# Optimization experiments

Hardware: AMD Instinct MI355X
Metric: run time of the kernel (lower is better)

Reference implementation:

```python
import jax, jax.numpy as jnp
import numpy as np

TIMESTEPS = 8
NUM_HEADS = 16
CTX = 1024
D = 1024
HD = D // NUM_HEADS
LN_EPS = 1e-5


def setup_inputs() -> dict:
    key = jax.random.key(0)
    ks = jax.random.split(key, 16)
    s = 0.02
    return {
        "current_embs": jax.random.normal(ks[0], (4, CTX, D), jnp.float32),
        "emb_table": jax.random.normal(ks[1], (TIMESTEPS, D), jnp.float32) * s,
        "Wq": jax.random.normal(ks[2], (NUM_HEADS, D, HD), jnp.float32) * s,
        "Wk": jax.random.normal(ks[3], (NUM_HEADS, D, HD), jnp.float32) * s,
        "Wv": jax.random.normal(ks[4], (NUM_HEADS, D, HD), jnp.float32) * s,
        "fc_w": jax.random.normal(ks[5], (D, D), jnp.float32) * s,
        "fc_b": jnp.zeros((D,), jnp.float32),
        "ln1_w": jnp.ones((D,), jnp.float32),
        "ln1_b": jnp.zeros((D,), jnp.float32),
        "ln2_w": jnp.ones((D,), jnp.float32),
        "ln2_b": jnp.zeros((D,), jnp.float32),
        "mlp_w1": jax.random.normal(ks[6], (D, 2 * D), jnp.float32) * s,
        "mlp_b1": jnp.zeros((2 * D,), jnp.float32),
        "mlp_w2": jax.random.normal(ks[7], (2 * D, D), jnp.float32) * s,
        "mlp_b2": jnp.zeros((D,), jnp.float32),
        "mlp_w3": jax.random.normal(ks[8], (D, D), jnp.float32) * s,
        "mlp_b3": jnp.zeros((D,), jnp.float32),
    }


def _layernorm(x, w, b):
    mu = jnp.mean(x, axis=-1, keepdims=True)
    var = jnp.var(x, axis=-1, keepdims=True)
    return (x - mu) * jax.lax.rsqrt(var + LN_EPS) * w + b


def _block(x, Wq, Wk, Wv, fc_w, fc_b, ln1_w, ln1_b, ln2_w, ln2_b,
           mlp_w1, mlp_b1, mlp_w2, mlp_b2, mlp_w3, mlp_b3):
    B, T, C = x.shape
    h = _layernorm(x, ln1_w, ln1_b)
    # per-head projections: [B,H,T,HD]
    q = jnp.einsum("btd,hdk->bhtk", h, Wq)
    k = jnp.einsum("btd,hdk->bhtk", h, Wk)
    v = jnp.einsum("btd,hdk->bhtk", h, Wv)
    # NOTE: original scales by embed_size**-0.5 (C), not head_dim**-0.5
    wei = jnp.einsum("bhtk,bhsk->bhts", q, k) * (C ** -0.5)
    causal = jnp.tril(jnp.ones((T, T), bool))
    wei = jnp.where(causal, wei, -jnp.inf)
    wei = jax.nn.softmax(wei, axis=-1)
    attn = jnp.einsum("bhts,bhsk->bhtk", wei, v)  # [B,H,T,HD]
    attn = attn.transpose(0, 2, 1, 3).reshape(B, T, C)  # concat heads
    sa = attn @ fc_w + fc_b
    x = x + sa  # dropout is identity in eval mode
    h2 = _layernorm(x, ln2_w, ln2_b)
    m = ((h2 @ mlp_w1 + mlp_b1) @ mlp_w2 + mlp_b2) @ mlp_w3 + mlp_b3
    m = jax.nn.gelu(m, approximate=False)  # GELU after three stacked Linears, as in source
    return x + m


def reference(current_embs, emb_table, Wq, Wk, Wv, fc_w, fc_b,
              ln1_w, ln1_b, ln2_w, ln2_b,
              mlp_w1, mlp_b1, mlp_w2, mlp_b2, mlp_w3, mlp_b3):
    new_embs = current_embs
    for i in range(TIMESTEPS):
        current_embs = current_embs + new_embs + emb_table[i][None, None, :]
        new_embs = _block(current_embs, Wq, Wk, Wv, fc_w, fc_b,
                          ln1_w, ln1_b, ln2_w, ln2_b,
                          mlp_w1, mlp_b1, mlp_w2, mlp_b2, mlp_w3, mlp_b3)
    return new_embs
```

## Files before the change

kernel.cpp:

```cpp
#include <hip/hip_runtime.h>
#include <hip/hip_bf16.h>
#include <math.h>

typedef __bf16 bf16;
typedef __bf16 bf16x8 __attribute__((ext_vector_type(8)));
typedef __bf16 bf16x4 __attribute__((ext_vector_type(4)));
typedef short  s16x4  __attribute__((ext_vector_type(4)));
typedef float  f32x4  __attribute__((ext_vector_type(4)));

#define MFMA32(a,b,c) __builtin_amdgcn_mfma_f32_16x16x32_bf16((a),(b),(c),0,0,0)
#define MFMA16(a,b,c) __builtin_amdgcn_mfma_f32_16x16x16bf16_1k((a),(b),(c),0,0,0)
#define EXP2F(x) __builtin_amdgcn_exp2f(x)
#define GLL16(gp, lp) __builtin_amdgcn_global_load_lds(\
    (const __attribute__((address_space(1))) void*)(gp), \
    (__attribute__((address_space(3))) void*)(lp), 16, 0, 0)

__device__ __forceinline__ float wave_sum(float v){
#pragma unroll
  for(int off=1; off<64; off<<=1) v += __shfl_xor(v, off);
  return v;
}

__global__ __launch_bounds__(256) void add_ln_kernel(
    const float* __restrict__ xsrc, const float* __restrict__ addsrc,
    const float* __restrict__ emb,
    const float* __restrict__ gw, const float* __restrict__ gb,
    float* __restrict__ xout, bf16* __restrict__ hout)
{
  const int row = blockIdx.x;
  const int t = threadIdx.x;
  const size_t rbase = (size_t)row * 1024;
  float4 x = ((const float4*)(xsrc + rbase))[t];
  if(addsrc){
    float4 a = ((const float4*)(addsrc + rbase))[t];
    x.x += a.x; x.y += a.y; x.z += a.z; x.w += a.w;
  }
  if(emb){
    float4 e = ((const float4*)emb)[t];
    x.x += e.x; x.y += e.y; x.z += e.z; x.w += e.w;
  }
  if(xout) ((float4*)(xout + rbase))[t] = x;

  float s = x.x + x.y + x.z + x.w;
  float q = x.x*x.x + x.y*x.y + x.z*x.z + x.w*x.w;
  s = wave_sum(s); q = wave_sum(q);
  __shared__ float red[8];
  const int w = t >> 6;
  if((t & 63) == 0){ red[w] = s; red[4+w] = q; }
  __syncthreads();
  s = red[0]+red[1]+red[2]+red[3];
  q = red[4]+red[5]+red[6]+red[7];
  const float mean = s * (1.0f/1024.0f);
  const float var  = q * (1.0f/1024.0f) - mean*mean;
  const float inv  = rsqrtf(var + 1e-5f);

  float4 wv = ((const float4*)gw)[t];
  float4 bv = ((const float4*)gb)[t];
  bf16x4 hv;
  hv[0] = (bf16)((x.x - mean)*inv*wv.x + bv.x);
  hv[1] = (bf16)((x.y - mean)*inv*wv.y + bv.y);
  hv[2] = (bf16)((x.z - mean)*inv*wv.z + bv.z);
  hv[3] = (bf16)((x.w - mean)*inv*wv.w + bv.w);
  *(bf16x4*)(hout + rbase + t*4) = hv;
}

__global__ __launch_bounds__(256) void pack_all_kernel(
    const float* __restrict__ Wq, const float* __restrict__ Wk, const float* __restrict__ Wv,
    const float* __restrict__ fcw, const float* __restrict__ w2,
    const float* __restrict__ w3,  const float* __restrict__ w1,
    bf16* __restrict__ wqkvT, bf16* __restrict__ fcT,
    bf16* __restrict__ w2T,   bf16* __restrict__ w3T, bf16* __restrict__ w1pl)
{
  const int bid = blockIdx.x;
  const int tid = threadIdx.x;
  if(bid >= 1792){
    const int i0 = (bid-1792)*2048 + tid*8;
    float4 a = *(const float4*)(w1 + i0);
    float4 b = *(const float4*)(w1 + i0 + 4);
    bf16x8 o;
    o[0]=(bf16)a.x; o[1]=(bf16)a.y; o[2]=(bf16)a.z; o[3]=(bf16)a.w;
    o[4]=(bf16)b.x; o[5]=(bf16)b.y; o[6]=(bf16)b.z; o[7]=(bf16)b.w;
    *(bf16x8*)(w1pl + i0) = o;
    return;
  }

  __shared__ float tile[64][65];
  const float* src; bf16* dst;
  int src_ld, dst_ld;
  if(bid < 768){
    const int seg = bid >> 8, r8 = bid & 255;
    const int h = r8 >> 4, d0 = (r8 & 15)*64;
    const float* W = (seg==0) ? Wq : (seg==1 ? Wk : Wv);
    src = W + h*65536 + (size_t)d0*64;  src_ld = 64;
    dst = wqkvT + ((size_t)(seg*1024 + h*64))*1024 + d0;  dst_ld = 1024;
  } else if(bid < 1024){
    const int t2 = bid - 768;
    const int k0 = (t2 >> 4)*64, n0 = (t2 & 15)*64;
    src = fcw + (size_t)k0*1024 + n0;  src_ld = 1024;
    dst = fcT + (size_t)n0*1024 + k0;  dst_ld = 1024;
  } else if(bid < 1536){
    const int t2 = bid - 1024;
    const int k0 = (t2 >> 4)*64, n0 = (t2 & 15)*64;
    src = w2 + (size_t)k0*1024 + n0;  src_ld = 1024;
    dst = w2T + (size_t)n0*2048 + k0;  dst_ld = 2048;
  } else {
    const int t2 = bid - 1536;
    const int k0 = (t2 >> 4)*64, n0 = (t2 & 15)*64;
    src = w3 + (size_t)k0*1024 + n0;  src_ld = 1024;
    dst = w3T + (size_t)n0*1024 + k0;  dst_ld = 1024;
  }

  {
    const int r = tid >> 4, c4 = (tid & 15)*4;
#pragma unroll
    for(int p=0; p<4; p++){
      float4 v = *(const float4*)(src + (size_t)(r + 16*p)*src_ld + c4);
      tile[r+16*p][c4]   = v.x;
      tile[r+16*p][c4+1] = v.y;
      tile[r+16*p][c4+2] = v.z;
      tile[r+16*p][c4+3] = v.w;
    }
  }
  __syncthreads();
  {
    const int n = tid >> 2, k16 = (tid & 3)*16;
#pragma unroll
    for(int half=0; half<2; half++){
      bf16x8 o;
#pragma unroll
      for(int j=0; j<8; j++) o[j] = (bf16)tile[k16 + half*8 + j][n];
      *(bf16x8*)(dst + (size_t)n*dst_ld + k16 + half*8) = o;
    }
  }
}

__global__ __launch_bounds__(256) void biasmv_kernel(const float* __restrict__ bin, const bf16* __restrict__ WT,
                                                     const float* __restrict__ badd, float* __restrict__ out, int Kd){
  const int n = blockIdx.x, t = threadIdx.x;
  float acc = 0.f;
  for(int k=t; k<Kd; k+=256) acc += bin[k]*(float)WT[(size_t)n*Kd + k];
  acc = wave_sum(acc);
  __shared__ float red[4];
  if((t&63)==0) red[t>>6] = acc;
  __syncthreads();
  if(t==0) out[n] = red[0]+red[1]+red[2]+red[3] + badd[n];
}

template<int EPI, int BLKM, int KH>
__global__ __launch_bounds__(256,2) void gemm_kernel(
    const bf16* __restrict__ A, const bf16* __restrict__ Bt,
    float* __restrict__ outf, bf16* __restrict__ outb,
    bf16* __restrict__ o2, bf16* __restrict__ o3,
    const float* __restrict__ bias, const float* __restrict__ res,
    const float* __restrict__ res2, const float* __restrict__ embn,
    int N, int K)
{
  constexpr int RM = BLKM/32;
  constexpr int HM = BLKM/2;
  constexpr int AISS = BLKM/32;
  __shared__ __align__(16) bf16 As[KH*BLKM*64];
  __shared__ __align__(16) bf16 Bs[KH*128*64];
  const int tid = threadIdx.x, w = tid>>6, lane = tid&63;
  const int quad = lane>>4, l16 = lane&15;
  const int wm = w&1, wn = w>>1;
  const int tn = blockIdx.x, tm = blockIdx.y;

  const int srow = lane>>3;
  const int sch  = (lane&7) ^ srow;
  const bf16* Ag = A  + (size_t)(tm*BLKM + w*8 + srow)*K + sch*8;
  const bf16* Bg = Bt + (size_t)(tn*128  + w*8 + srow)*K + sch*8;

  f32x4 acc[RM][4] = {};

  for(int k0 = 0; k0 < K; k0 += 64*KH){
#pragma unroll
    for(int h=0; h<KH; h++){
#pragma unroll
      for(int i=0;i<AISS;i++) GLL16(Ag + h*64 + (size_t)(i*32)*K, As + h*(BLKM*64) + (w*8 + i*32)*64);
#pragma unroll
      for(int i=0;i<4;i++)    GLL16(Bg + h*64 + (size_t)(i*32)*K, Bs + h*(128*64) + (w*8 + i*32)*64);
    }
    Ag += 64*KH; Bg += 64*KH;
    __syncthreads();
#pragma unroll
    for(int h=0; h<KH; h++){
      const bf16* Ash = As + h*(BLKM*64);
      const bf16* Bsh = Bs + h*(128*64);
      bf16x8 af[RM][2], bfr[4][2];
#pragma unroll
      for(int r=0;r<RM;r++){
        const int row = wm*HM + r*16 + l16;
        const bf16* rp = Ash + row*64;
#pragma unroll
        for(int kc=0;kc<2;kc++)
          af[r][kc] = *(const bf16x8*)(rp + ((kc*4+quad) ^ (row&7))*8);
      }
#pragma unroll
      for(int c=0;c<4;c++){
        const int row = wn*64 + c*16 + l16;
        const bf16* rp = Bsh + row*64;
#pragma unroll
        for(int kc=0;kc<2;kc++)
          bfr[c][kc] = *(const bf16x8*)(rp + ((kc*4+quad) ^ (row&7))*8);
      }
#pragma unroll
      for(int kc=0;kc<2;kc++)
#pragma unroll
        for(int r=0;r<RM;r++)
#pragma unroll
          for(int c=0;c<4;c++)
            acc[r][c] = MFMA32(af[r][kc], bfr[c][kc], acc[r][c]);
    }
    __syncthreads();
  }

#pragma unroll
  for(int r=0;r<RM;r++){
    const int grow0 = tm*BLKM + wm*HM + r*16 + quad*4;
#pragma unroll
    for(int c=0;c<4;c++){
      const int gcol = tn*128 + wn*64 + c*16 + l16;
      float bv = 0.0f;
      if constexpr (EPI>=1 && EPI!=4) bv = bias[gcol];
      if constexpr (EPI==4){
        const int seg = gcol >> 10;
        if(seg < 2){
          bf16* op = (seg==0) ? outb : o2;
          const float qs = (seg==0) ? 0.045084439f : 1.0f;
          const int col = gcol & 1023;
#pragma unroll
          for(int g=0; g<4; g++)
            op[(size_t)(grow0+g)*1024 + col] = (bf16)(acc[r][c][g]*qs);
        } else {
          const int col0 = gcol & 1023, hh = col0>>6, kk = col0&63;
          const int btok = grow0>>10, t0 = grow0&1023;
          bf16x4 pv;
#pragma unroll
          for(int g=0; g<4; g++) pv[g] = (bf16)acc[r][c][g];
          *(bf16x4*)(o3 + ((size_t)(btok*16+hh)*64 + kk)*1024 + t0) = pv;
        }
      } else {
        const float ev = (EPI==5) ? embn[gcol] : 0.0f;
#pragma unroll
        for(int g=0; g<4; g++){
          const float vv = acc[r][c][g] + bv;
          const size_t idx = (size_t)(grow0+g)*N + gcol;
          if constexpr (EPI<=1){
            outb[idx] = (bf16)vv;
          } else if constexpr (EPI==2){
            outf[idx] = res[idx] + vv;
          } else if constexpr (EPI==3){
            const float gel = 0.5f*vv*(1.0f + erff(vv*0.70710678118654752f));
            outf[idx] = res[idx] + gel;
          } else {
            const float gel = 0.5f*vv*(1.0f + erff(vv*0.70710678118654752f));
            outf[idx] = res[idx] + gel + res2[idx] + ev;
          }
        }
      }
    }
  }
}

constexpr int KSZ = 64*64;

__global__ __launch_bounds__(256,4) void attn_kernel(
    const bf16* __restrict__ Q, const bf16* __restrict__ Km,
    const bf16* __restrict__ Vt, bf16* __restrict__ O)
{
  __shared__ __align__(16) bf16 Ks[2*KSZ];
  __shared__ __align__(16) bf16 Vs[2*KSZ];
  const int qt = (int)((0xCDEF98BA67453210ull >> (blockIdx.y*4)) & 15);
  const int bh = blockIdx.x;
  const int b = bh >> 4, h = bh & 15;
  const int tid = threadIdx.x;
  const int w = tid>>6, lane = tid&63, quad = lane>>4, l16 = lane&15;
  const size_t qbase = (size_t)b*1024*1024 + (size_t)h*64;
  const size_t vbase = (size_t)(bh*64)*1024;
  const int qrow0 = qt*64 + w*16;
  const int myrow = qrow0 + l16;

  const bf16* qp = Q + qbase + (size_t)myrow*1024 + quad*8;
  bf16x8 bq0 = *(const bf16x8*)qp, bq1 = *(const bf16x8*)(qp + 32);

  f32x4 o[4] = {};
  float l = 0.f;
  const f32x4 zf = {0.f,0.f,0.f,0.f};

  const bf16* kg = Km + qbase + (size_t)(w*8 + (lane>>3))*1024 + ((lane&7)^(lane>>3))*8;
  const bf16* vg = Vt + vbase + (size_t)(w*8 + (lane>>3))*1024 + ((lane&7)^(lane>>3))*8;

  GLL16(kg,                       Ks + w*512);
  GLL16(kg + (size_t)32*1024,     Ks + 2048 + w*512);
  GLL16(vg,                       Vs + w*512);
  GLL16(vg + (size_t)32*1024,     Vs + 2048 + w*512);

  for(int kb = 0; kb <= qt; kb++){
    const int cur = kb & 1;
    __syncthreads();

    if(kb < qt){
      const bf16* kgp = kg + (size_t)(kb+1)*64*1024;
      const bf16* vgp = vg + (size_t)(kb+1)*64;
      bf16* kd = Ks + (cur^1)*KSZ + w*512;
      bf16* vd = Vs + (cur^1)*KSZ + w*512;
      GLL16(kgp,                   kd);
      GLL16(kgp + (size_t)32*1024, kd + 2048);
      GLL16(vgp,                   vd);
      GLL16(vgp + (size_t)32*1024, vd + 2048);
    }

    const bool diag = (kb == qt);
    const int nc = diag ? (w+1) : 4;
    const bf16* ksb = Ks + cur*KSZ;
    const bf16* vsb = Vs + cur*KSZ;

    f32x4 s[4];
#pragma unroll
    for(int c=0;c<4;c++){
      if(c >= nc) continue;
      const int row = c*16 + l16;
      const bf16* rp = ksb + row*64;
      bf16x8 ak0 = *(const bf16x8*)(rp + (( quad      ^ (row&7))<<3));
      bf16x8 ak1 = *(const bf16x8*)(rp + (((quad^4)   ^ (row&7))<<3));
      s[c] = MFMA32(ak0, bq0, zf);
      s[c] = MFMA32(ak1, bq1, s[c]);
    }

    s16x4 pp[4];
#pragma unroll
    for(int c=0;c<4;c++){
      if(c >= nc) continue;
      bf16x4 pb;
#pragma unroll
      for(int g=0;g<4;g++){
        const int key = kb*64 + c*16 + quad*4 + g;
        const float e = (diag && key > myrow) ? 0.f : EXP2F(s[c][g]);
        l += e; pb[g] = (bf16)e;
      }
      pp[c] = __builtin_bit_cast(s16x4, pb);
    }

#pragma unroll
    for(int c=0;c<4;c++){
      if(c >= nc) continue;
#pragma unroll
      for(int d=0;d<4;d++){
        const int row = d*16 + l16;
        const int eo  = ((((c*2 + (quad>>1)) ^ (row&7))<<3) + ((quad&1)<<2));
        bf16x4 av = *(const bf16x4*)(vsb + row*64 + eo);
        o[d] = MFMA16(__builtin_bit_cast(s16x4, av), pp[c], o[d]);
      }
    }
  }

  l += __shfl_xor(l, 16); l += __shfl_xor(l, 32);

  __syncthreads();
  {
    bf16* ot = Ks + w*(16*72);
    const float inv = 1.0f / l;
#pragma unroll
    for(int d=0;d<4;d++)
#pragma unroll
      for(int g=0;g<4;g++)
        ot[l16*72 + d*16 + quad*4 + g] = (bf16)(o[d][g]*inv);
#pragma unroll
    for(int p2=0;p2<2;p2++){
      const int qr = (lane>>3) + 8*p2, hd0 = (lane&7)*8;
      bf16x8 val = *(const bf16x8*)(ot + qr*72 + hd0);
      *(bf16x8*)(O + qbase + (size_t)(qrow0+qr)*1024 + hd0) = val;
    }
  }
}

extern "C" void kernel_launch(void* const* d_in, const int* in_sizes, int n_in,
                              void* d_out, int out_size, void* d_ws, size_t ws_size,
                              hipStream_t stream)
{
  const float* x_in = (const float*)d_in[0];
  const float* emb  = (const float*)d_in[1];
  const float* Wq   = (const float*)d_in[2];
  const float* Wk   = (const float*)d_in[3];
  const float* Wv   = (const float*)d_in[4];
  const float* fcw  = (const float*)d_in[5];
  const float* fcb  = (const float*)d_in[6];
  const float* ln1w = (const float*)d_in[7];
  const float* ln1b = (const float*)d_in[8];
  const float* ln2w = (const float*)d_in[9];
  const float* ln2b = (const float*)d_in[10];
  const float* w1   = (const float*)d_in[11];
  const float* b1   = (const float*)d_in[12];
  const float* w2   = (const float*)d_in[13];
  const float* b2   = (const float*)d_in[14];
  const float* w3   = (const float*)d_in[15];
  const float* b3   = (const float*)d_in[16];

  char* ws = (char*)d_ws;
  const size_t MB = 1024*1024;
  float* cur    = (float*)(ws + 0);
  float* x1     = (float*)(ws + 16*MB);
  bf16*  hb     = (bf16*)(ws + 48*MB);
  bf16*  attnb  = (bf16*)(ws + 56*MB);
  bf16*  qb     = (bf16*)(ws + 64*MB);
  bf16*  kbuf   = (bf16*)(ws + 72*MB);
  bf16*  vtb    = (bf16*)(ws + 80*MB);
  bf16*  w1pl   = (bf16*)(ws + 88*MB);
  bf16*  T12    = (bf16*)(ws + 92*MB);
  bf16*  wqkvT  = (bf16*)(ws + 96*MB);
  bf16*  fcT    = (bf16*)(ws + 102*MB);
  bf16*  w2T    = (bf16*)(ws + 104*MB);
  bf16*  w3T    = (bf16*)(ws + 108*MB);
  bf16*  WeffT  = (bf16*)(ws + 110*MB);
  float* tmpb   = (float*)(ws + 112*MB);
  float* beff   = (float*)(ws + 112*MB + 8192);

  pack_all_kernel<<<2816,256,0,stream>>>(Wq, Wk, Wv, fcw, w2, w3, w1,
                                         wqkvT, fcT, w2T, w3T, w1pl);
  gemm_kernel<0,64,2><<<dim3(8,16),256,0,stream>>>(w1pl, w2T, nullptr, T12,   nullptr, nullptr, nullptr, nullptr, nullptr, nullptr, 1024, 2048);
  gemm_kernel<0,64,2><<<dim3(8,16),256,0,stream>>>(w3T,  T12, nullptr, WeffT, nullptr, nullptr, nullptr, nullptr, nullptr, nullptr, 1024, 1024);
  biasmv_kernel<<<1024,256,0,stream>>>(b1,   w2T, b2, tmpb, 2048);
  biasmv_kernel<<<1024,256,0,stream>>>(tmpb, w3T, b3, beff, 1024);

  add_ln_kernel<<<4096,256,0,stream>>>(x_in, x_in, emb, ln1w, ln1b, cur, hb);
  for(int t=0; t<8; t++){
    if(t > 0)
      add_ln_kernel<<<4096,256,0,stream>>>(cur, nullptr, nullptr, ln1w, ln1b, nullptr, hb);
    gemm_kernel<4,128,1><<<dim3(24,32),256,0,stream>>>(hb, wqkvT, nullptr, qb, kbuf, vtb, nullptr, nullptr, nullptr, nullptr, 3072, 1024);
    attn_kernel<<<dim3(64,16),256,0,stream>>>(qb, kbuf, vtb, attnb);
    gemm_kernel<2,64,2><<<dim3(8,64),256,0,stream>>>(attnb, fcT, x1, nullptr, nullptr, nullptr, fcb, cur, nullptr, nullptr, 1024, 1024);
    add_ln_kernel<<<4096,256,0,stream>>>(x1, nullptr, nullptr, ln2w, ln2b, nullptr, hb);
    if(t < 7)
      gemm_kernel<5,64,2><<<dim3(8,64),256,0,stream>>>(hb, WeffT, cur, nullptr, nullptr, nullptr, beff, x1, cur, emb + (t+1)*1024, 1024, 1024);
    else
      gemm_kernel<3,64,2><<<dim3(8,64),256,0,stream>>>(hb, WeffT, (float*)d_out, nullptr, nullptr, nullptr, beff, x1, nullptr, nullptr, 1024, 1024);
  }
}
```

Before: 1.003 ms.

## Compute LayerNorm row statistics in GEMM epilogues via atomics, split LN kernel

The residual-producing GEMM epilogues now accumulate per-row sum and sum-of-squares and add them into a stats buffer with atomicAdd. The LayerNorm kernels only normalize using those precomputed stats, which removes the block reduction from the LN pass. The intent is to shorten the LN kernels' critical path. The cost is extra shuffles and atomics in the GEMM epilogue, plus a zeroing kernel for the stats buffer. The LN kernel still re-reads x, so memory traffic is about the same, and computing variance as E[x²]−mean² in fp32 is less numerically robust.

```diff
diff --git a/kernel.cpp b/kernel.cpp
--- a/kernel.cpp
+++ b/kernel.cpp
@@ -21,25 +21,18 @@
   return v;
 }
 
-__global__ __launch_bounds__(256) void add_ln_kernel(
-    const float* __restrict__ xsrc, const float* __restrict__ addsrc,
-    const float* __restrict__ emb,
-    const float* __restrict__ gw, const float* __restrict__ gb,
-    float* __restrict__ xout, bf16* __restrict__ hout)
+__global__ __launch_bounds__(256) void add_stats_kernel(
+    const float* __restrict__ xsrc, const float* __restrict__ emb,
+    float* __restrict__ xout, float* __restrict__ ostats)
 {
   const int row = blockIdx.x;
   const int t = threadIdx.x;
   const size_t rbase = (size_t)row * 1024;
   float4 x = ((const float4*)(xsrc + rbase))[t];
-  if(addsrc){
-    float4 a = ((const float4*)(addsrc + rbase))[t];
-    x.x += a.x; x.y += a.y; x.z += a.z; x.w += a.w;
-  }
-  if(emb){
-    float4 e = ((const float4*)emb)[t];
-    x.x += e.x; x.y += e.y; x.z += e.z; x.w += e.w;
-  }
-  if(xout) ((float4*)(xout + rbase))[t] = x;
+  float4 e = ((const float4*)emb)[t];
+  x.x = 2.0f*x.x + e.x; x.y = 2.0f*x.y + e.y;
+  x.z = 2.0f*x.z + e.z; x.w = 2.0f*x.w + e.w;
+  ((float4*)(xout + rbase))[t] = x;
 
   float s = x.x + x.y + x.z + x.w;
   float q = x.x*x.x + x.y*x.y + x.z*x.z + x.w*x.w;
@@ -48,19 +41,35 @@
   const int w = t >> 6;
   if((t & 63) == 0){ red[w] = s; red[4+w] = q; }
   __syncthreads();
-  s = red[0]+red[1]+red[2]+red[3];
-  q = red[4]+red[5]+red[6]+red[7];
-  const float mean = s * (1.0f/1024.0f);
-  const float var  = q * (1.0f/1024.0f) - mean*mean;
+  if(t == 0){
+    ostats[row]        = red[0]+red[1]+red[2]+red[3];
+    ostats[4096 + row] = red[4]+red[5]+red[6]+red[7];
+  }
+}
+
+__global__ __launch_bounds__(256) void zero_kernel(float* __restrict__ p){
+  ((float4*)p)[blockIdx.x*256 + threadIdx.x] = float4{0.f,0.f,0.f,0.f};
+}
+
+__global__ __launch_bounds__(256) void norm_ln_kernel(
+    const float* __restrict__ x, const float* __restrict__ stats,
+    const float* __restrict__ gw, const float* __restrict__ gb,
+    bf16* __restrict__ hout)
+{
+  const int row = blockIdx.x;
+  const int t = threadIdx.x;
+  const size_t rbase = (size_t)row * 1024;
+  float4 xv = ((const float4*)(x + rbase))[t];
+  const float mean = stats[row] * (1.0f/1024.0f);
+  const float var  = stats[4096+row] * (1.0f/1024.0f) - mean*mean;
   const float inv  = rsqrtf(var + 1e-5f);
-
   float4 wv = ((const float4*)gw)[t];
   float4 bv = ((const float4*)gb)[t];
   bf16x4 hv;
-  hv[0] = (bf16)((x.x - mean)*inv*wv.x + bv.x);
-  hv[1] = (bf16)((x.y - mean)*inv*wv.y + bv.y);
-  hv[2] = (bf16)((x.z - mean)*inv*wv.z + bv.z);
-  hv[3] = (bf16)((x.w - mean)*inv*wv.w + bv.w);
+  hv[0] = (bf16)((xv.x - mean)*inv*wv.x + bv.x);
+  hv[1] = (bf16)((xv.y - mean)*inv*wv.y + bv.y);
+  hv[2] = (bf16)((xv.z - mean)*inv*wv.z + bv.z);
+  hv[3] = (bf16)((xv.w - mean)*inv*wv.w + bv.w);
   *(bf16x4*)(hout + rbase + t*4) = hv;
 }
 
@@ -153,7 +162,7 @@
     bf16* __restrict__ o2, bf16* __restrict__ o3,
     const float* __restrict__ bias, const float* __restrict__ res,
     const float* __restrict__ res2, const float* __restrict__ embn,
-    int N, int K)
+    float* __restrict__ ostats, int N, int K)
 {
   constexpr int RM = BLKM/32;
   constexpr int HM = BLKM/2;
@@ -214,6 +223,7 @@
     __syncthreads();
   }
 
+  float rs[RM][4] = {}, rq[RM][4] = {};
 #pragma unroll
   for(int r=0;r<RM;r++){
     const int grow0 = tm*BLKM + wm*HM + r*16 + quad*4;
@@ -248,17 +258,38 @@
           if constexpr (EPI<=1){
             outb[idx] = (bf16)vv;
           } else if constexpr (EPI==2){
-            outf[idx] = res[idx] + vv;
+            const float ov = res[idx] + vv;
+            outf[idx] = ov;
+            rs[r][g] += ov; rq[r][g] += ov*ov;
           } else if constexpr (EPI==3){
             const float gel = 0.5f*vv*(1.0f + erff(vv*0.70710678118654752f));
             outf[idx] = res[idx] + gel;
           } else {
             const float gel = 0.5f*vv*(1.0f + erff(vv*0.70710678118654752f));
-            outf[idx] = res[idx] + gel + res2[idx] + ev;
+            const float ov = res[idx] + gel + res2[idx] + ev;
+            outf[idx] = ov;
+            rs[r][g] += ov; rq[r][g] += ov*ov;
           }
         }
       }
     }
+  }
+  if constexpr (EPI==2 || EPI==5){
+#pragma unroll
+    for(int r=0;r<RM;r++)
+#pragma unroll
+      for(int g=0;g<4;g++){
+        float s1 = rs[r][g], s2 = rq[r][g];
+        s1 += __shfl_xor(s1,1); s2 += __shfl_xor(s2,1);
+        s1 += __shfl_xor(s1,2); s2 += __shfl_xor(s2,2);
+        s1 += __shfl_xor(s1,4); s2 += __shfl_xor(s2,4);
+        s1 += __shfl_xor(s1,8); s2 += __shfl_xor(s2,8);
+        if(l16 == 0){
+          const int row = tm*BLKM + wm*HM + r*16 + quad*4 + g;
+          atomicAdd(ostats + row, s1);
+          atomicAdd(ostats + 4096 + row, s2);
+        }
+      }
   }
 }
 
@@ -414,25 +445,29 @@
   bf16*  WeffT  = (bf16*)(ws + 110*MB);
   float* tmpb   = (float*)(ws + 112*MB);
   float* beff   = (float*)(ws + 112*MB + 8192);
-
+  float* statsb = (float*)(ws + 113*MB);
+
+  zero_kernel<<<128,256,0,stream>>>(statsb);
   pack_all_kernel<<<2816,256,0,stream>>>(Wq, Wk, Wv, fcw, w2, w3, w1,
                                          wqkvT, fcT, w2T, w3T, w1pl);
-  gemm_kernel<0,64,2><<<dim3(8,16),256,0,stream>>>(w1pl, w2T, nullptr, T12,   nullptr, nullptr, nullptr, nullptr, nullptr, nullptr, 1024, 2048);
-  gemm_kernel<0,64,2><<<dim3(8,16),256,0,stream>>>(w3T,  T12, nullptr, WeffT, nullptr, nullptr, nullptr, nullptr, nullptr, nullptr, 1024, 1024);
+  gemm_kernel<0,64,2><<<dim3(8,16),256,0,stream>>>(w1pl, w2T, nullptr, T12,   nullptr, nullptr, nullptr, nullptr, nullptr, nullptr, nullptr, 1024, 2048);
+  gemm_kernel<0,64,2><<<dim3(8,16),256,0,stream>>>(w3T,  T12, nullptr, WeffT, nullptr, nullptr, nullptr, nullptr, nullptr, nullptr, nullptr, 1024, 1024);
   biasmv_kernel<<<1024,256,0,stream>>>(b1,   w2T, b2, tmpb, 2048);
   biasmv_kernel<<<1024,256,0,stream>>>(tmpb, w3T, b3, beff, 1024);
 
-  add_ln_kernel<<<4096,256,0,stream>>>(x_in, x_in, emb, ln1w, ln1b, cur, hb);
+  add_stats_kernel<<<4096,256,0,stream>>>(x_in, emb, cur, statsb);
   for(int t=0; t<8; t++){
-    if(t > 0)
-      add_ln_kernel<<<4096,256,0,stream>>>(cur, nullptr, nullptr, ln1w, ln1b, nullptr, hb);
-    gemm_kernel<4,128,1><<<dim3(24,32),256,0,stream>>>(hb, wqkvT, nullptr, qb, kbuf, vtb, nullptr, nullptr, nullptr, nullptr, 3072, 1024);
+    float* s1  = statsb + (size_t)(2*t  )*8192;
+    float* s2  = statsb + (size_t)(2*t+1)*8192;
+    float* s1n = statsb + (size_t)(2*t+2)*8192;
+    norm_ln_kernel<<<4096,256,0,stream>>>(cur, s1, ln1w, ln1b, hb);
+    gemm_kernel<4,128,1><<<dim3(24,32),256,0,stream>>>(hb, wqkvT, nullptr, qb, kbuf, vtb, nullptr, nullptr, nullptr, nullptr, nullptr, 3072, 1024);
     attn_kernel<<<dim3(64,16),256,0,stream>>>(qb, kbuf, vtb, attnb);
-    gemm_kernel<2,64,2><<<dim3(8,64),256,0,stream>>>(attnb, fcT, x1, nullptr, nullptr, nullptr, fcb, cur, nullptr, nullptr, 1024, 1024);
-    add_ln_kernel<<<4096,256,0,stream>>>(x1, nullptr, nullptr, ln2w, ln2b, nullptr, hb);
+    gemm_kernel<2,64,2><<<dim3(8,64),256,0,stream>>>(attnb, fcT, x1, nullptr, nullptr, nullptr, fcb, cur, nullptr, nullptr, s2, 1024, 1024);
+    norm_ln_kernel<<<4096,256,0,stream>>>(x1, s2, ln2w, ln2b, hb);
     if(t < 7)
-      gemm_kernel<5,64,2><<<dim3(8,64),256,0,stream>>>(hb, WeffT, cur, nullptr, nullptr, nullptr, beff, x1, cur, emb + (t+1)*1024, 1024, 1024);
+      gemm_kernel<5,64,2><<<dim3(8,64),256,0,stream>>>(hb, WeffT, cur, nullptr, nullptr, nullptr, beff, x1, cur, emb + (t+1)*1024, s1n, 1024, 1024);
     else
-      gemm_kernel<3,64,2><<<dim3(8,64),256,0,stream>>>(hb, WeffT, (float*)d_out, nullptr, nullptr, nullptr, beff, x1, nullptr, nullptr, 1024, 1024);
-  }
-}
+      gemm_kernel<3,64,2><<<dim3(8,64),256,0,stream>>>(hb, WeffT, (float*)d_out, nullptr, nullptr, nullptr, beff, x1, nullptr, nullptr, nullptr, 1024, 1024);
+  }
+}
```

New measurement: 1.031 ms. 1.03x slower.
